# Kernel optimization log

Measured on AMD Instinct MI355X. Metric: run time of the kernel, lower is better.

## Reference

```python
import jax, jax.numpy as jnp
import numpy as np

N = 50000      # nodes
E = 800000     # edges (avg degree 16)
IN, H, OUT = 128, 128, 64
NEG_SLOPE = 0.01  # F.leaky_relu default


def _glorot(key, shape):
    lim = float(np.sqrt(6.0 / (shape[0] + shape[1])))
    return jax.random.uniform(key, shape, jnp.float32, -lim, lim)


def setup_inputs() -> dict:
    key = jax.random.key(0)
    ks = jax.random.split(key, 12)
    x = jax.random.normal(ks[0], (N, IN), jnp.float32)
    edge_index = jax.random.randint(ks[1], (2, E), 0, N, dtype=jnp.int64)
    edge_weight = jax.random.uniform(ks[2], (E,), jnp.float32)
    params = {}
    dims = [(IN, H), (H, H), (H, H), (H, OUT)]
    for i, (di, do) in enumerate(dims, start=1):
        params[f"W{i}"] = _glorot(ks[2 + i], (di, do))
        params[f"b{i}"] = jnp.zeros((do,), jnp.float32)
    return {"x": x, "edge_index": edge_index, "edge_weight": edge_weight, **params}


def _gcn_norm(edge_index, edge_weight, n):
    # PyG gcn_norm: add self-loops with weight 1, symmetric D^-1/2 A D^-1/2
    loop = jnp.arange(n, dtype=edge_index.dtype)
    row = jnp.concatenate([edge_index[0], loop])   # source
    col = jnp.concatenate([edge_index[1], loop])   # target
    w = jnp.concatenate([edge_weight, jnp.ones((n,), edge_weight.dtype)])
    deg = jax.ops.segment_sum(w, col, num_segments=n)
    dinv = jnp.where(deg > 0, jax.lax.rsqrt(deg), 0.0)
    norm = dinv[row] * w * dinv[col]
    return row, col, norm


def _gcn_conv(x, W, b, row, col, norm, n):
    h = x @ W                                   # [N, out] dense GEMM
    msg = h[row] * norm[:, None]                # gather + edge scale  [E+N, out]
    out = jax.ops.segment_sum(msg, col, num_segments=n)  # scatter-add
    return out + b


def reference(x, edge_index, edge_weight, W1, b1, W2, b2, W3, b3, W4, b4):
    n = x.shape[0]
    row, col, norm = _gcn_norm(edge_index, edge_weight, n)  # identical for all layers
    h = _gcn_conv(x, W1, b1, row, col, norm, n)
    h = jax.nn.leaky_relu(h, NEG_SLOPE)
    # dropout (p=0.25) is identity in eval mode
    h = _gcn_conv(h, W2, b2, row, col, norm, n)
    h = jax.nn.leaky_relu(h, NEG_SLOPE)
    h = _gcn_conv(h, W3, b3, row, col, norm, n)
    h = jax.nn.leaky_relu(h, NEG_SLOPE)
    h = _gcn_conv(h, W4, b4, row, col, norm, n)
    return h
```

## Files before the change

kernel.cpp:

```cpp
#include <hip/hip_runtime.h>
#include <hip/hip_bf16.h>


#define CAP 64


__global__ void fillcap_k(const int* __restrict__ ei, const float* __restrict__ ew,
                          int* __restrict__ fillc, int* __restrict__ src,
                          float* __restrict__ nrmv, int E) {
    int e = blockIdx.x * 256 + threadIdx.x;
    if (e >= E) return;
    int r = ei[e];
    int c = ei[E + e];
    int pos = atomicAdd(&fillc[c], 1);
    if (pos < CAP) {
        src[c * CAP + pos] = r;
        nrmv[c * CAP + pos] = ew[e];
    }
}

__global__ void segdeg_k(const int* __restrict__ fillc, const float* __restrict__ nrmv,
                         float* __restrict__ dinv, int n) {
    int t = blockIdx.x * 256 + threadIdx.x;
    int node = t >> 4, l = t & 15;
    if (node >= n) return;
    int len = min(fillc[node], CAP);
    float s = 0.f;
    for (int i = l; i < len; i += 16) s += nrmv[node * CAP + i];
    #pragma unroll
    for (int d = 1; d < 16; d <<= 1) s += __shfl_xor(s, d);
    if (l == 0) dinv[node] = rsqrtf(s + 1.0f);
}

__global__ void nrmfix_k(const int* __restrict__ fillc, const int* __restrict__ src,
                         const float* __restrict__ dinv, float* __restrict__ nrmv, int n) {
    int t = blockIdx.x * 256 + threadIdx.x;
    int node = t >> 4, l = t & 15;
    if (node >= n) return;
    int len = min(fillc[node], CAP);
    float dc = dinv[node];
    for (int i = l; i < len; i += 16) {
        int idx = node * CAP + i;
        nrmv[idx] = dinv[src[idx]] * nrmv[idx] * dc;
    }
}


template <bool LEAKY>
__global__ __launch_bounds__(256) void aggcap128_k(
        const float* __restrict__ h, const int* __restrict__ fillc,
        const int* __restrict__ src, const float* __restrict__ nrmv,
        const float* __restrict__ dinv, const float* __restrict__ bias,
        float* __restrict__ out, int n) {
    int node = blockIdx.x * 4 + (threadIdx.x >> 6);
    if (node >= n) return;
    int lane = threadIdx.x & 63;
    int beg = node * CAP;
    int len = min(fillc[node], CAP);
    float2 acc = make_float2(0.f, 0.f);
    int e = 0;
    for (; e + 8 <= len; e += 8) {
        int s0 = src[beg+e+0], s1 = src[beg+e+1], s2 = src[beg+e+2], s3 = src[beg+e+3];
        int s4 = src[beg+e+4], s5 = src[beg+e+5], s6 = src[beg+e+6], s7 = src[beg+e+7];
        float w0 = nrmv[beg+e+0], w1 = nrmv[beg+e+1], w2 = nrmv[beg+e+2], w3 = nrmv[beg+e+3];
        float w4 = nrmv[beg+e+4], w5 = nrmv[beg+e+5], w6 = nrmv[beg+e+6], w7 = nrmv[beg+e+7];
        float2 v0 = *(const float2*)&h[(size_t)s0 * 128 + lane * 2];
        float2 v1 = *(const float2*)&h[(size_t)s1 * 128 + lane * 2];
        float2 v2 = *(const float2*)&h[(size_t)s2 * 128 + lane * 2];
        float2 v3 = *(const float2*)&h[(size_t)s3 * 128 + lane * 2];
        float2 v4 = *(const float2*)&h[(size_t)s4 * 128 + lane * 2];
        float2 v5 = *(const float2*)&h[(size_t)s5 * 128 + lane * 2];
        float2 v6 = *(const float2*)&h[(size_t)s6 * 128 + lane * 2];
        float2 v7 = *(const float2*)&h[(size_t)s7 * 128 + lane * 2];
        acc.x += w0*v0.x; acc.y += w0*v0.y;
        acc.x += w1*v1.x; acc.y += w1*v1.y;
        acc.x += w2*v2.x; acc.y += w2*v2.y;
        acc.x += w3*v3.x; acc.y += w3*v3.y;
        acc.x += w4*v4.x; acc.y += w4*v4.y;
        acc.x += w5*v5.x; acc.y += w5*v5.y;
        acc.x += w6*v6.x; acc.y += w6*v6.y;
        acc.x += w7*v7.x; acc.y += w7*v7.y;
    }
    for (; e < len; ++e) {
        int s = src[beg + e];
        float w = nrmv[beg + e];
        float2 hv = *(const float2*)&h[(size_t)s * 128 + lane * 2];
        acc.x += w * hv.x;
        acc.y += w * hv.y;
    }
    float di = dinv[node];
    float ws = di * di;
    float2 hv = *(const float2*)&h[(size_t)node * 128 + lane * 2];
    acc.x += ws * hv.x;
    acc.y += ws * hv.y;
    float2 bb = *(const float2*)&bias[lane * 2];
    acc.x += bb.x;
    acc.y += bb.y;
    if (LEAKY) {
        acc.x = acc.x > 0.f ? acc.x : 0.01f * acc.x;
        acc.y = acc.y > 0.f ? acc.y : 0.01f * acc.y;
    }
    *(float2*)&out[(size_t)node * 128 + lane * 2] = acc;
}

__global__ __launch_bounds__(256) void aggcap64_k(
        const float* __restrict__ h, const int* __restrict__ fillc,
        const int* __restrict__ src, const float* __restrict__ nrmv,
        const float* __restrict__ dinv, const float* __restrict__ bias,
        float* __restrict__ out, int n) {
    int node = blockIdx.x * 4 + (threadIdx.x >> 6);
    if (node >= n) return;
    int lane = threadIdx.x & 63;
    int beg = node * CAP;
    int len = min(fillc[node], CAP);
    float acc = 0.f;
    int e = 0;
    for (; e + 8 <= len; e += 8) {
        int s0 = src[beg+e+0], s1 = src[beg+e+1], s2 = src[beg+e+2], s3 = src[beg+e+3];
        int s4 = src[beg+e+4], s5 = src[beg+e+5], s6 = src[beg+e+6], s7 = src[beg+e+7];
        float w0 = nrmv[beg+e+0], w1 = nrmv[beg+e+1], w2 = nrmv[beg+e+2], w3 = nrmv[beg+e+3];
        float w4 = nrmv[beg+e+4], w5 = nrmv[beg+e+5], w6 = nrmv[beg+e+6], w7 = nrmv[beg+e+7];
        float v0 = h[(size_t)s0 * 64 + lane];
        float v1 = h[(size_t)s1 * 64 + lane];
        float v2 = h[(size_t)s2 * 64 + lane];
        float v3 = h[(size_t)s3 * 64 + lane];
        float v4 = h[(size_t)s4 * 64 + lane];
        float v5 = h[(size_t)s5 * 64 + lane];
        float v6 = h[(size_t)s6 * 64 + lane];
        float v7 = h[(size_t)s7 * 64 + lane];
        acc += w0*v0 + w1*v1 + w2*v2 + w3*v3 + w4*v4 + w5*v5 + w6*v6 + w7*v7;
    }
    for (; e < len; ++e) {
        acc += nrmv[beg + e] * h[(size_t)src[beg + e] * 64 + lane];
    }
    float di = dinv[node];
    acc += di * di * h[(size_t)node * 64 + lane];
    acc += bias[lane];
    out[(size_t)node * 64 + lane] = acc;
}


template <int OUTD>
__global__ __launch_bounds__(512) void gemm_k(const float* __restrict__ A,
                                              const float* __restrict__ W,
                                              float* __restrict__ C, int nrows) {
    constexpr int CW = OUTD / 16;
    constexpr int WF4 = (32 * OUTD / 4) / 512;
    __shared__ float As[32][132];
    __shared__ float Ws[32][OUTD];
    const int t = threadIdx.x;
    const int rowbase = blockIdx.x * 128;
    const int tx = t & 15, ty = t >> 4;
    const int r0 = ty * 4, c0 = tx * CW;

    float acc[4][CW];
    #pragma unroll
    for (int i = 0; i < 4; ++i)
        #pragma unroll
        for (int j = 0; j < CW; ++j) acc[i][j] = 0.f;

    const int arow0 = t >> 3, akq0 = t & 7;
    const int arow1 = (t + 512) >> 3, akq1 = t & 7;

    auto loadA = [&](int kt, int row, int kq) -> float4 {
        int gr = rowbase + row;
        if (gr < nrows) return *(const float4*)&A[(size_t)gr * 128 + kt * 32 + kq * 4];
        return make_float4(0.f, 0.f, 0.f, 0.f);
    };
    auto stA = [&](int row, int kq, float4 v) {
        As[kq * 4 + 0][row] = v.x;
        As[kq * 4 + 1][row] = v.y;
        As[kq * 4 + 2][row] = v.z;
        As[kq * 4 + 3][row] = v.w;
    };

    stA(arow0, akq0, loadA(0, arow0, akq0));
    stA(arow1, akq1, loadA(0, arow1, akq1));
    #pragma unroll
    for (int u = 0; u < WF4; ++u) {
        int idx = t + u * 512;
        int k = idx / (OUTD / 4), cq = idx % (OUTD / 4);
        *(float4*)&Ws[k][cq * 4] = *(const float4*)&W[(size_t)k * OUTD + cq * 4];
    }
    __syncthreads();

    float4 pa0, pa1, pw[WF4];
    #pragma unroll
    for (int kt = 0; kt < 4; ++kt) {
        if (kt < 3) {
            pa0 = loadA(kt + 1, arow0, akq0);
            pa1 = loadA(kt + 1, arow1, akq1);
            #pragma unroll
            for (int u = 0; u < WF4; ++u) {
                int idx = t + u * 512;
                int k = idx / (OUTD / 4), cq = idx % (OUTD / 4);
                pw[u] = *(const float4*)&W[(size_t)((kt + 1) * 32 + k) * OUTD + cq * 4];
            }
        }
        #pragma unroll 8
        for (int k = 0; k < 32; ++k) {
            float4 a = *(const float4*)&As[k][r0];
            float w[CW];
            #pragma unroll
            for (int j = 0; j < CW; j += 4)
                *(float4*)&w[j] = *(const float4*)&Ws[k][c0 + j];
            #pragma unroll
            for (int j = 0; j < CW; ++j) {
                acc[0][j] += a.x * w[j];
                acc[1][j] += a.y * w[j];
                acc[2][j] += a.z * w[j];
                acc[3][j] += a.w * w[j];
            }
        }
        __syncthreads();
        if (kt < 3) {
            stA(arow0, akq0, pa0);
            stA(arow1, akq1, pa1);
            #pragma unroll
            for (int u = 0; u < WF4; ++u) {
                int idx = t + u * 512;
                int k = idx / (OUTD / 4), cq = idx % (OUTD / 4);
                *(float4*)&Ws[k][cq * 4] = pw[u];
            }
            __syncthreads();
        }
    }

    #pragma unroll
    for (int i = 0; i < 4; ++i) {
        int gr = rowbase + r0 + i;
        if (gr < nrows) {
            #pragma unroll
            for (int j = 0; j < CW; j += 4)
                *(float4*)&C[(size_t)gr * OUTD + c0 + j] = *(float4*)&acc[i][j];
        }
    }
}


__global__ void deg_cnt_k(const int* __restrict__ ei, const float* __restrict__ ew,
                          float* __restrict__ deg, int* __restrict__ cnt, int E) {
    int e = blockIdx.x * 256 + threadIdx.x;
    if (e >= E) return;
    int c = ei[E + e];
    atomicAdd(&deg[c], ew[e]);
    atomicAdd(&cnt[c], 1);
}

__global__ void dinv_k(float* __restrict__ d, int n) {
    int i = blockIdx.x * 256 + threadIdx.x;
    if (i >= n) return;
    d[i] = rsqrtf(d[i] + 1.0f);
}

__global__ void scan_blocks_k(const int* __restrict__ cnt, int* __restrict__ rowptr,
                              int* __restrict__ partials, int n) {
    int gid = blockIdx.x * 1024 + threadIdx.x;
    int v = (gid < n) ? cnt[gid] : 0;
    int lane = threadIdx.x & 63, wid = threadIdx.x >> 6;
    int x = v;
    #pragma unroll
    for (int d = 1; d < 64; d <<= 1) {
        int y = __shfl_up(x, d);
        if (lane >= d) x += y;
    }
    __shared__ int wsum[16];
    if (lane == 63) wsum[wid] = x;
    __syncthreads();
    if (wid == 0 && lane < 16) {
        int s = wsum[lane];
        #pragma unroll
        for (int d = 1; d < 16; d <<= 1) {
            int y = __shfl_up(s, d);
            if (lane >= d) s += y;
        }
        wsum[lane] = s;
    }
    __syncthreads();
    int inc = x + (wid > 0 ? wsum[wid - 1] : 0);
    if (gid < n) rowptr[gid] = inc - v;
    if (threadIdx.x == 1023) partials[blockIdx.x] = inc;
}

__global__ void scan_part_k(int* __restrict__ p, int nb) {
    int lane = threadIdx.x;
    int v = (lane < nb) ? p[lane] : 0;
    int x = v;
    #pragma unroll
    for (int d = 1; d < 64; d <<= 1) {
        int y = __shfl_up(x, d);
        if (lane >= d) x += y;
    }
    if (lane < nb) p[lane] = x - v;
    if (lane == 63) p[nb] = x;
}

__global__ void scan_add_k(int* __restrict__ rowptr, const int* __restrict__ p,
                           int n, int nb) {
    int i = blockIdx.x * 1024 + threadIdx.x;
    if (i < n) rowptr[i] += p[blockIdx.x];
    if (i == 0) rowptr[n] = p[nb];
}

__global__ void fill_k(const int* __restrict__ ei, const float* __restrict__ ew,
                       const float* __restrict__ dinv, const int* __restrict__ rowptr,
                       int* __restrict__ fillc, int* __restrict__ src,
                       float* __restrict__ nrm, int E) {
    int e = blockIdx.x * 256 + threadIdx.x;
    if (e >= E) return;
    int r = ei[e];
    int c = ei[E + e];
    int pos = rowptr[c] + atomicAdd(&fillc[c], 1);
    src[pos] = r;
    nrm[pos] = dinv[r] * ew[e] * dinv[c];
}

template <bool LEAKY>
__global__ __launch_bounds__(256) void agg128_k(
        const float* __restrict__ h, const int* __restrict__ rowptr,
        const int* __restrict__ src, const float* __restrict__ nrm,
        const float* __restrict__ dinv, const float* __restrict__ bias,
        float* __restrict__ out, int n) {
    int node = blockIdx.x * 4 + (threadIdx.x >> 6);
    if (node >= n) return;
    int lane = threadIdx.x & 63;
    int beg = rowptr[node], end = rowptr[node + 1];
    float2 acc = make_float2(0.f, 0.f);
    int e = beg;
    for (; e + 4 <= end; e += 4) {
        int s0 = src[e], s1 = src[e + 1], s2 = src[e + 2], s3 = src[e + 3];
        float w0 = nrm[e], w1 = nrm[e + 1], w2 = nrm[e + 2], w3 = nrm[e + 3];
        float2 v0 = *(const float2*)&h[(size_t)s0 * 128 + lane * 2];
        float2 v1 = *(const float2*)&h[(size_t)s1 * 128 + lane * 2];
        float2 v2 = *(const float2*)&h[(size_t)s2 * 128 + lane * 2];
        float2 v3 = *(const float2*)&h[(size_t)s3 * 128 + lane * 2];
        acc.x += w0 * v0.x; acc.y += w0 * v0.y;
        acc.x += w1 * v1.x; acc.y += w1 * v1.y;
        acc.x += w2 * v2.x; acc.y += w2 * v2.y;
        acc.x += w3 * v3.x; acc.y += w3 * v3.y;
    }
    for (; e < end; ++e) {
        int s = src[e];
        float w = nrm[e];
        float2 hv = *(const float2*)&h[(size_t)s * 128 + lane * 2];
        acc.x += w * hv.x;
        acc.y += w * hv.y;
    }
    float di = dinv[node];
    float ws = di * di;
    float2 hv = *(const float2*)&h[(size_t)node * 128 + lane * 2];
    acc.x += ws * hv.x;
    acc.y += ws * hv.y;
    float2 bb = *(const float2*)&bias[lane * 2];
    acc.x += bb.x;
    acc.y += bb.y;
    if (LEAKY) {
        acc.x = acc.x > 0.f ? acc.x : 0.01f * acc.x;
        acc.y = acc.y > 0.f ? acc.y : 0.01f * acc.y;
    }
    *(float2*)&out[(size_t)node * 128 + lane * 2] = acc;
}

__global__ __launch_bounds__(256) void agg64_k(
        const float* __restrict__ h, const int* __restrict__ rowptr,
        const int* __restrict__ src, const float* __restrict__ nrm,
        const float* __restrict__ dinv, const float* __restrict__ bias,
        float* __restrict__ out, int n) {
    int node = blockIdx.x * 4 + (threadIdx.x >> 6);
    if (node >= n) return;
    int lane = threadIdx.x & 63;
    int beg = rowptr[node], end = rowptr[node + 1];
    float acc = 0.f;
    int e = beg;
    for (; e + 4 <= end; e += 4) {
        int s0 = src[e], s1 = src[e + 1], s2 = src[e + 2], s3 = src[e + 3];
        float w0 = nrm[e], w1 = nrm[e + 1], w2 = nrm[e + 2], w3 = nrm[e + 3];
        acc += w0 * h[(size_t)s0 * 64 + lane];
        acc += w1 * h[(size_t)s1 * 64 + lane];
        acc += w2 * h[(size_t)s2 * 64 + lane];
        acc += w3 * h[(size_t)s3 * 64 + lane];
    }
    for (; e < end; ++e) {
        acc += nrm[e] * h[(size_t)src[e] * 64 + lane];
    }
    float di = dinv[node];
    acc += di * di * h[(size_t)node * 64 + lane];
    acc += bias[lane];
    out[(size_t)node * 64 + lane] = acc;
}


extern "C" void kernel_launch(void* const* d_in, const int* in_sizes, int n_in,
                              void* d_out, int out_size, void* d_ws, size_t ws_size,
                              hipStream_t stream) {
    const float* x  = (const float*)d_in[0];
    const int* ei   = (const int*)d_in[1];
    const float* ew = (const float*)d_in[2];
    const float* W1 = (const float*)d_in[3];
    const float* b1 = (const float*)d_in[4];
    const float* W2 = (const float*)d_in[5];
    const float* b2 = (const float*)d_in[6];
    const float* W3 = (const float*)d_in[7];
    const float* b3 = (const float*)d_in[8];
    const float* W4 = (const float*)d_in[9];
    const float* b4 = (const float*)d_in[10];

    const int N = in_sizes[0] / 128;
    const int E = in_sizes[1] / 2;

    auto alignup = [](size_t o) { return (o + 255) & ~(size_t)255; };
    char* ws = (char*)d_ws;
    (void)n_in; (void)out_size;

    int eb = (E + 255) / 256;
    int gb = (N + 127) / 128;
    int ab = (N + 3) / 4;
    int qb = (N * 16 + 255) / 256;

    size_t off = 0;
    float* dinv  = (float*)(ws + off); off = alignup(off + (size_t)N * 4);
    int*   fillc = (int*)(ws + off);   off = alignup(off + (size_t)N * 4);
    size_t zb_cap = off;
    int*   srcC  = (int*)(ws + off);   off = alignup(off + (size_t)N * CAP * 4);
    float* nrmC  = (float*)(ws + off); off = alignup(off + (size_t)N * CAP * 4);
    float* hbufC = (float*)(ws + off); off = alignup(off + (size_t)N * 128 * 4);
    float* featC = (float*)(ws + off); off = alignup(off + (size_t)N * 128 * 4);
    size_t need_cap = off;

    if (need_cap <= ws_size) {
        hipMemsetAsync(d_ws, 0, zb_cap, stream);
        fillcap_k<<<eb, 256, 0, stream>>>(ei, ew, fillc, srcC, nrmC, E);
        segdeg_k<<<qb, 256, 0, stream>>>(fillc, nrmC, dinv, N);
        nrmfix_k<<<qb, 256, 0, stream>>>(fillc, srcC, dinv, nrmC, N);

        gemm_k<128><<<gb, 512, 0, stream>>>(x, W1, hbufC, N);
        aggcap128_k<true><<<ab, 256, 0, stream>>>(hbufC, fillc, srcC, nrmC, dinv, b1, featC, N);
        gemm_k<128><<<gb, 512, 0, stream>>>(featC, W2, hbufC, N);
        aggcap128_k<true><<<ab, 256, 0, stream>>>(hbufC, fillc, srcC, nrmC, dinv, b2, featC, N);
        gemm_k<128><<<gb, 512, 0, stream>>>(featC, W3, hbufC, N);
        aggcap128_k<true><<<ab, 256, 0, stream>>>(hbufC, fillc, srcC, nrmC, dinv, b3, featC, N);
        gemm_k<64><<<gb, 512, 0, stream>>>(featC, W4, hbufC, N);
        aggcap64_k<<<ab, 256, 0, stream>>>(hbufC, fillc, srcC, nrmC, dinv, b4, (float*)d_out, N);
        return;
    }

    off = 0;
    float* deg   = (float*)(ws + off); off = alignup(off + (size_t)N * 4);
    int*   cnt   = (int*)(ws + off);   off = alignup(off + (size_t)N * 4);
    int*   fillc2= (int*)(ws + off);   off = alignup(off + (size_t)N * 4);
    size_t zbytes = off;
    int*   rowptr = (int*)(ws + off);  off = alignup(off + (size_t)(N + 1) * 4);
    int*   parts  = (int*)(ws + off);  off = alignup(off + 64 * 4);
    int*   srcA   = (int*)(ws + off);  off = alignup(off + (size_t)E * 4);
    float* nrm    = (float*)(ws + off); off = alignup(off + (size_t)E * 4);
    float* hbuf   = (float*)(ws + off); off = alignup(off + (size_t)N * 128 * 4);
    float* feat   = (float*)(ws + off); off = alignup(off + (size_t)N * 128 * 4);

    hipMemsetAsync(d_ws, 0, zbytes, stream);

    int nb = (N + 255) / 256;
    int sb = (N + 1023) / 1024;

    deg_cnt_k<<<eb, 256, 0, stream>>>(ei, ew, deg, cnt, E);
    dinv_k<<<nb, 256, 0, stream>>>(deg, N);
    scan_blocks_k<<<sb, 1024, 0, stream>>>(cnt, rowptr, parts, N);
    scan_part_k<<<1, 64, 0, stream>>>(parts, sb);
    scan_add_k<<<sb, 1024, 0, stream>>>(rowptr, parts, N, sb);
    fill_k<<<eb, 256, 0, stream>>>(ei, ew, deg, rowptr, fillc2, srcA, nrm, E);

    gemm_k<128><<<gb, 512, 0, stream>>>(x, W1, hbuf, N);
    agg128_k<true><<<ab, 256, 0, stream>>>(hbuf, rowptr, srcA, nrm, deg, b1, feat, N);
    gemm_k<128><<<gb, 512, 0, stream>>>(feat, W2, hbuf, N);
    agg128_k<true><<<ab, 256, 0, stream>>>(hbuf, rowptr, srcA, nrm, deg, b2, feat, N);
    gemm_k<128><<<gb, 512, 0, stream>>>(feat, W3, hbuf, N);
    agg128_k<true><<<ab, 256, 0, stream>>>(hbuf, rowptr, srcA, nrm, deg, b3, feat, N);
    gemm_k<64><<<gb, 512, 0, stream>>>(feat, W4, hbuf, N);
    agg64_k<<<ab, 256, 0, stream>>>(hbuf, rowptr, srcA, nrm, deg, b4, (float*)d_out, N);
}
```

Before: 398.6 us.

## Pack edge src and norm into int2 and split wavefront across edges with float4 gathers

Source index and normalised weight are now stored together as one int2 per edge slot, so each edge needs one load instead of two. The aggregation kernels now split each wavefront into halves (or quarters for 64-wide features). Each sub-group gathers a different edge using float4 loads, and the partial sums are combined with cross-lane shuffles at the end. This aims to issue fewer, wider memory requests and to overlap more independent gathers. The cost is extra shuffle reductions and idle lanes during the final store.

After: 377.9 us. 1.05x faster.

```diff
diff --git a/kernel.cpp b/kernel.cpp
--- a/kernel.cpp
+++ b/kernel.cpp
@@ -6,42 +6,41 @@
 
 
 __global__ void fillcap_k(const int* __restrict__ ei, const float* __restrict__ ew,
-                          int* __restrict__ fillc, int* __restrict__ src,
-                          float* __restrict__ nrmv, int E) {
+                          int* __restrict__ fillc, int2* __restrict__ ed, int E) {
     int e = blockIdx.x * 256 + threadIdx.x;
     if (e >= E) return;
     int r = ei[e];
     int c = ei[E + e];
     int pos = atomicAdd(&fillc[c], 1);
     if (pos < CAP) {
-        src[c * CAP + pos] = r;
-        nrmv[c * CAP + pos] = ew[e];
-    }
-}
-
-__global__ void segdeg_k(const int* __restrict__ fillc, const float* __restrict__ nrmv,
+        ed[(size_t)c * CAP + pos] = make_int2(r, __float_as_int(ew[e]));
+    }
+}
+
+__global__ void segdeg_k(const int* __restrict__ fillc, const int2* __restrict__ ed,
                          float* __restrict__ dinv, int n) {
     int t = blockIdx.x * 256 + threadIdx.x;
     int node = t >> 4, l = t & 15;
     if (node >= n) return;
     int len = min(fillc[node], CAP);
     float s = 0.f;
-    for (int i = l; i < len; i += 16) s += nrmv[node * CAP + i];
+    for (int i = l; i < len; i += 16) s += __int_as_float(ed[(size_t)node * CAP + i].y);
     #pragma unroll
     for (int d = 1; d < 16; d <<= 1) s += __shfl_xor(s, d);
     if (l == 0) dinv[node] = rsqrtf(s + 1.0f);
 }
 
-__global__ void nrmfix_k(const int* __restrict__ fillc, const int* __restrict__ src,
-                         const float* __restrict__ dinv, float* __restrict__ nrmv, int n) {
+__global__ void nrmfix_k(const int* __restrict__ fillc, int2* __restrict__ ed,
+                         const float* __restrict__ dinv, int n) {
     int t = blockIdx.x * 256 + threadIdx.x;
     int node = t >> 4, l = t & 15;
     if (node >= n) return;
     int len = min(fillc[node], CAP);
     float dc = dinv[node];
     for (int i = l; i < len; i += 16) {
-        int idx = node * CAP + i;
-        nrmv[idx] = dinv[src[idx]] * nrmv[idx] * dc;
+        size_t idx = (size_t)node * CAP + i;
+        int2 d = ed[idx];
+        ((float*)&ed[idx])[1] = dinv[d.x] * __int_as_float(d.y) * dc;
     }
 }
 
@@ -49,94 +48,117 @@
 template <bool LEAKY>
 __global__ __launch_bounds__(256) void aggcap128_k(
         const float* __restrict__ h, const int* __restrict__ fillc,
-        const int* __restrict__ src, const float* __restrict__ nrmv,
-        const float* __restrict__ dinv, const float* __restrict__ bias,
-        float* __restrict__ out, int n) {
+        const int2* __restrict__ ed, const float* __restrict__ dinv,
+        const float* __restrict__ bias, float* __restrict__ out, int n) {
     int node = blockIdx.x * 4 + (threadIdx.x >> 6);
     if (node >= n) return;
     int lane = threadIdx.x & 63;
-    int beg = node * CAP;
+    int half = lane >> 5;
+    int q = lane & 31;
+    size_t beg = (size_t)node * CAP;
     int len = min(fillc[node], CAP);
-    float2 acc = make_float2(0.f, 0.f);
+    float4 acc = make_float4(0.f, 0.f, 0.f, 0.f);
     int e = 0;
     for (; e + 8 <= len; e += 8) {
-        int s0 = src[beg+e+0], s1 = src[beg+e+1], s2 = src[beg+e+2], s3 = src[beg+e+3];
-        int s4 = src[beg+e+4], s5 = src[beg+e+5], s6 = src[beg+e+6], s7 = src[beg+e+7];
-        float w0 = nrmv[beg+e+0], w1 = nrmv[beg+e+1], w2 = nrmv[beg+e+2], w3 = nrmv[beg+e+3];
-        float w4 = nrmv[beg+e+4], w5 = nrmv[beg+e+5], w6 = nrmv[beg+e+6], w7 = nrmv[beg+e+7];
-        float2 v0 = *(const float2*)&h[(size_t)s0 * 128 + lane * 2];
-        float2 v1 = *(const float2*)&h[(size_t)s1 * 128 + lane * 2];
-        float2 v2 = *(const float2*)&h[(size_t)s2 * 128 + lane * 2];
-        float2 v3 = *(const float2*)&h[(size_t)s3 * 128 + lane * 2];
-        float2 v4 = *(const float2*)&h[(size_t)s4 * 128 + lane * 2];
-        float2 v5 = *(const float2*)&h[(size_t)s5 * 128 + lane * 2];
-        float2 v6 = *(const float2*)&h[(size_t)s6 * 128 + lane * 2];
-        float2 v7 = *(const float2*)&h[(size_t)s7 * 128 + lane * 2];
-        acc.x += w0*v0.x; acc.y += w0*v0.y;
-        acc.x += w1*v1.x; acc.y += w1*v1.y;
-        acc.x += w2*v2.x; acc.y += w2*v2.y;
-        acc.x += w3*v3.x; acc.y += w3*v3.y;
-        acc.x += w4*v4.x; acc.y += w4*v4.y;
-        acc.x += w5*v5.x; acc.y += w5*v5.y;
-        acc.x += w6*v6.x; acc.y += w6*v6.y;
-        acc.x += w7*v7.x; acc.y += w7*v7.y;
-    }
-    for (; e < len; ++e) {
-        int s = src[beg + e];
-        float w = nrmv[beg + e];
-        float2 hv = *(const float2*)&h[(size_t)s * 128 + lane * 2];
-        acc.x += w * hv.x;
-        acc.y += w * hv.y;
-    }
+        int2 d0 = ed[beg + e + 0 + half];
+        int2 d1 = ed[beg + e + 2 + half];
+        int2 d2 = ed[beg + e + 4 + half];
+        int2 d3 = ed[beg + e + 6 + half];
+        float4 v0 = *(const float4*)&h[(size_t)d0.x * 128 + q * 4];
+        float4 v1 = *(const float4*)&h[(size_t)d1.x * 128 + q * 4];
+        float4 v2 = *(const float4*)&h[(size_t)d2.x * 128 + q * 4];
+        float4 v3 = *(const float4*)&h[(size_t)d3.x * 128 + q * 4];
+        float w0 = __int_as_float(d0.y), w1 = __int_as_float(d1.y);
+        float w2 = __int_as_float(d2.y), w3 = __int_as_float(d3.y);
+        acc.x += w0*v0.x; acc.y += w0*v0.y; acc.z += w0*v0.z; acc.w += w0*v0.w;
+        acc.x += w1*v1.x; acc.y += w1*v1.y; acc.z += w1*v1.z; acc.w += w1*v1.w;
+        acc.x += w2*v2.x; acc.y += w2*v2.y; acc.z += w2*v2.z; acc.w += w2*v2.w;
+        acc.x += w3*v3.x; acc.y += w3*v3.y; acc.z += w3*v3.z; acc.w += w3*v3.w;
+    }
+    if (e < len) {
+        #pragma unroll
+        for (int t = 0; t < 4; ++t) {
+            int j = e + 2 * t + half;
+            bool ok = j < len;
+            int2 d = ed[beg + (ok ? j : 0)];
+            float w = ok ? __int_as_float(d.y) : 0.f;
+            int sr = ok ? d.x : node;
+            float4 v = *(const float4*)&h[(size_t)sr * 128 + q * 4];
+            acc.x += w*v.x; acc.y += w*v.y; acc.z += w*v.z; acc.w += w*v.w;
+        }
+    }
+    acc.x += __shfl_xor(acc.x, 32);
+    acc.y += __shfl_xor(acc.y, 32);
+    acc.z += __shfl_xor(acc.z, 32);
+    acc.w += __shfl_xor(acc.w, 32);
     float di = dinv[node];
     float ws = di * di;
-    float2 hv = *(const float2*)&h[(size_t)node * 128 + lane * 2];
-    acc.x += ws * hv.x;
-    acc.y += ws * hv.y;
-    float2 bb = *(const float2*)&bias[lane * 2];
-    acc.x += bb.x;
-    acc.y += bb.y;
+    float4 hv = *(const float4*)&h[(size_t)node * 128 + q * 4];
+    float4 bb = *(const float4*)&bias[q * 4];
+    acc.x += ws*hv.x + bb.x;
+    acc.y += ws*hv.y + bb.y;
+    acc.z += ws*hv.z + bb.z;
+    acc.w += ws*hv.w + bb.w;
     if (LEAKY) {
         acc.x = acc.x > 0.f ? acc.x : 0.01f * acc.x;
         acc.y = acc.y > 0.f ? acc.y : 0.01f * acc.y;
-    }
-    *(float2*)&out[(size_t)node * 128 + lane * 2] = acc;
+        acc.z = acc.z > 0.f ? acc.z : 0.01f * acc.z;
+        acc.w = acc.w > 0.f ? acc.w : 0.01f * acc.w;
+    }
+    if (half == 0) *(float4*)&out[(size_t)node * 128 + q * 4] = acc;
 }
 
 __global__ __launch_bounds__(256) void aggcap64_k(
         const float* __restrict__ h, const int* __restrict__ fillc,
-        const int* __restrict__ src, const float* __restrict__ nrmv,
-        const float* __restrict__ dinv, const float* __restrict__ bias,
-        float* __restrict__ out, int n) {
+        const int2* __restrict__ ed, const float* __restrict__ dinv,
+        const float* __restrict__ bias, float* __restrict__ out, int n) {
     int node = blockIdx.x * 4 + (threadIdx.x >> 6);
     if (node >= n) return;
     int lane = threadIdx.x & 63;
-    int beg = node * CAP;
+    int qtr = lane >> 4;
+    int q = lane & 15;
+    size_t beg = (size_t)node * CAP;
     int len = min(fillc[node], CAP);
-    float acc = 0.f;
+    float4 acc = make_float4(0.f, 0.f, 0.f, 0.f);
     int e = 0;
     for (; e + 8 <= len; e += 8) {
-        int s0 = src[beg+e+0], s1 = src[beg+e+1], s2 = src[beg+e+2], s3 = src[beg+e+3];
-        int s4 = src[beg+e+4], s5 = src[beg+e+5], s6 = src[beg+e+6], s7 = src[beg+e+7];
-        float w0 = nrmv[beg+e+0], w1 = nrmv[beg+e+1], w2 = nrmv[beg+e+2], w3 = nrmv[beg+e+3];
-        float w4 = nrmv[beg+e+4], w5 = nrmv[beg+e+5], w6 = nrmv[beg+e+6], w7 = nrmv[beg+e+7];
-        float v0 = h[(size_t)s0 * 64 + lane];
-        float v1 = h[(size_t)s1 * 64 + lane];
-        float v2 = h[(size_t)s2 * 64 + lane];
-        float v3 = h[(size_t)s3 * 64 + lane];
-        float v4 = h[(size_t)s4 * 64 + lane];
-        float v5 = h[(size_t)s5 * 64 + lane];
-        float v6 = h[(size_t)s6 * 64 + lane];
-        float v7 = h[(size_t)s7 * 64 + lane];
-        acc += w0*v0 + w1*v1 + w2*v2 + w3*v3 + w4*v4 + w5*v5 + w6*v6 + w7*v7;
-    }
-    for (; e < len; ++e) {
-        acc += nrmv[beg + e] * h[(size_t)src[beg + e] * 64 + lane];
-    }
+        int2 d0 = ed[beg + e + 0 + qtr];
+        int2 d1 = ed[beg + e + 4 + qtr];
+        float4 v0 = *(const float4*)&h[(size_t)d0.x * 64 + q * 4];
+        float4 v1 = *(const float4*)&h[(size_t)d1.x * 64 + q * 4];
+        float w0 = __int_as_float(d0.y), w1 = __int_as_float(d1.y);
+        acc.x += w0*v0.x; acc.y += w0*v0.y; acc.z += w0*v0.z; acc.w += w0*v0.w;
+        acc.x += w1*v1.x; acc.y += w1*v1.y; acc.z += w1*v1.z; acc.w += w1*v1.w;
+    }
+    if (e < len) {
+        #pragma unroll
+        for (int t = 0; t < 2; ++t) {
+            int j = e + 4 * t + qtr;
+            bool ok = j < len;
+            int2 d = ed[beg + (ok ? j : 0)];
+            float w = ok ? __int_as_float(d.y) : 0.f;
+            int sr = ok ? d.x : node;
+            float4 v = *(const float4*)&h[(size_t)sr * 64 + q * 4];
+            acc.x += w*v.x; acc.y += w*v.y; acc.z += w*v.z; acc.w += w*v.w;
+        }
+    }
+    acc.x += __shfl_xor(acc.x, 16);
+    acc.y += __shfl_xor(acc.y, 16);
+    acc.z += __shfl_xor(acc.z, 16);
+    acc.w += __shfl_xor(acc.w, 16);
+    acc.x += __shfl_xor(acc.x, 32);
+    acc.y += __shfl_xor(acc.y, 32);
+    acc.z += __shfl_xor(acc.z, 32);
+    acc.w += __shfl_xor(acc.w, 32);
     float di = dinv[node];
-    acc += di * di * h[(size_t)node * 64 + lane];
-    acc += bias[lane];
-    out[(size_t)node * 64 + lane] = acc;
+    float ws = di * di;
+    float4 hv = *(const float4*)&h[(size_t)node * 64 + q * 4];
+    float4 bb = *(const float4*)&bias[q * 4];
+    acc.x += ws*hv.x + bb.x;
+    acc.y += ws*hv.y + bb.y;
+    acc.z += ws*hv.z + bb.z;
+    acc.w += ws*hv.w + bb.w;
+    if (qtr == 0) *(float4*)&out[(size_t)node * 64 + q * 4] = acc;
 }
 
 
@@ -421,26 +443,25 @@
     float* dinv  = (float*)(ws + off); off = alignup(off + (size_t)N * 4);
     int*   fillc = (int*)(ws + off);   off = alignup(off + (size_t)N * 4);
     size_t zb_cap = off;
-    int*   srcC  = (int*)(ws + off);   off = alignup(off + (size_t)N * CAP * 4);
-    float* nrmC  = (float*)(ws + off); off = alignup(off + (size_t)N * CAP * 4);
+    int2*  ed    = (int2*)(ws + off);  off = alignup(off + (size_t)N * CAP * 8);
     float* hbufC = (float*)(ws + off); off = alignup(off + (size_t)N * 128 * 4);
     float* featC = (float*)(ws + off); off = alignup(off + (size_t)N * 128 * 4);
     size_t need_cap = off;
 
     if (need_cap <= ws_size) {
         hipMemsetAsync(d_ws, 0, zb_cap, stream);
-        fillcap_k<<<eb, 256, 0, stream>>>(ei, ew, fillc, srcC, nrmC, E);
-        segdeg_k<<<qb, 256, 0, stream>>>(fillc, nrmC, dinv, N);
-        nrmfix_k<<<qb, 256, 0, stream>>>(fillc, srcC, dinv, nrmC, N);
+        fillcap_k<<<eb, 256, 0, stream>>>(ei, ew, fillc, ed, E);
+        segdeg_k<<<qb, 256, 0, stream>>>(fillc, ed, dinv, N);
+        nrmfix_k<<<qb, 256, 0, stream>>>(fillc, ed, dinv, N);
 
         gemm_k<128><<<gb, 512, 0, stream>>>(x, W1, hbufC, N);
-        aggcap128_k<true><<<ab, 256, 0, stream>>>(hbufC, fillc, srcC, nrmC, dinv, b1, featC, N);
+        aggcap128_k<true><<<ab, 256, 0, stream>>>(hbufC, fillc, ed, dinv, b1, featC, N);
         gemm_k<128><<<gb, 512, 0, stream>>>(featC, W2, hbufC, N);
-        aggcap128_k<true><<<ab, 256, 0, stream>>>(hbufC, fillc, srcC, nrmC, dinv, b2, featC, N);
+        aggcap128_k<true><<<ab, 256, 0, stream>>>(hbufC, fillc, ed, dinv, b2, featC, N);
         gemm_k<128><<<gb, 512, 0, stream>>>(featC, W3, hbufC, N);
-        aggcap128_k<true><<<ab, 256, 0, stream>>>(hbufC, fillc, srcC, nrmC, dinv, b3, featC, N);
+        aggcap128_k<true><<<ab, 256, 0, stream>>>(hbufC, fillc, ed, dinv, b3, featC, N);
         gemm_k<64><<<gb, 512, 0, stream>>>(featC, W4, hbufC, N);
-        aggcap64_k<<<ab, 256, 0, stream>>>(hbufC, fillc, srcC, nrmC, dinv, b4, (float*)d_out, N);
+        aggcap64_k<<<ab, 256, 0, stream>>>(hbufC, fillc, ed, dinv, b4, (float*)d_out, N);
         return;
     }
 
```
